# Performance work log

Hardware: AMD Instinct MI355X
Metric: run time of the kernel (lower is better)

The kernel has to match this reference:

```python
import jax, jax.numpy as jnp
import numpy as np

N_NODES = 50000
N_EDGES = 600000
D_FEAT = 128
HIDDEN = 128
N_CLASSES = 40
K_HOPS = 2


def setup_inputs() -> dict:
    key = jax.random.key(0)
    k_x, k_e, k_w1, k_b1, k_w2, k_b2 = jax.random.split(key, 6)
    x = jax.random.normal(k_x, (N_NODES, D_FEAT), dtype=jnp.float32)
    edge_index = jax.random.randint(k_e, (2, N_EDGES), 0, N_NODES, dtype=jnp.int64)
    # SGConv linear (applied after K-hop propagation) and classifier, Glorot-ish init
    W_sgc = jax.random.normal(k_w1, (D_FEAT, HIDDEN), dtype=jnp.float32) / np.sqrt(D_FEAT)
    b_sgc = jnp.zeros((HIDDEN,), dtype=jnp.float32)
    W_cls = jax.random.normal(k_w2, (HIDDEN, N_CLASSES), dtype=jnp.float32) / np.sqrt(HIDDEN)
    b_cls = jnp.zeros((N_CLASSES,), dtype=jnp.float32)
    return {"x": x, "edge_index": edge_index, "W_sgc": W_sgc, "b_sgc": b_sgc,
            "W_cls": W_cls, "b_cls": b_cls}


def _gcn_norm(edge_index, num_nodes):
    # Add self-loops (PyG SGConv default), compute symmetric GCN normalization.
    loops = jnp.arange(num_nodes, dtype=edge_index.dtype)
    src = jnp.concatenate([edge_index[0], loops])  # [E+N]
    dst = jnp.concatenate([edge_index[1], loops])  # [E+N]
    deg = jax.ops.segment_sum(jnp.ones_like(dst, dtype=jnp.float32), dst,
                              num_segments=num_nodes)
    dinv = jnp.where(deg > 0, jax.lax.rsqrt(deg), 0.0)
    norm = dinv[src] * dinv[dst]  # [E+N]
    return src, dst, norm


def reference(x, edge_index, W_sgc, b_sgc, W_cls, b_cls):
    num_nodes = x.shape[0]
    src, dst, norm = _gcn_norm(edge_index, num_nodes)
    h = x
    for _ in range(K_HOPS):  # K-hop propagation: h <- D^-1/2 (A+I) D^-1/2 h
        h = jax.ops.segment_sum(norm[:, None] * h[src], dst, num_segments=num_nodes)
    h = h @ W_sgc + b_sgc          # SGConv's trailing linear
    # F.dropout with training=False is identity (inference); skip.
    out = h @ W_cls + b_cls        # classifier
    return out
```

## Files before the change

### kernel.cpp

```cpp
#include <hip/hip_runtime.h>
#include <hip/hip_fp16.h>

#define N_NODES 50000
#define N_EDGES 600000
#define D 128
#define NC 40
#define BUCKET_CAP 48
#define NPART 8
#define PART_SZ (N_NODES / NPART)
#define E4 (N_EDGES / 4)
#define E4H (E4 / 2)
#define FUSE_ELEMS (D * NC + NC)

#define ZERO_BLKS ((N_NODES / 4 + 255) / 256)
#define FUSE_BLKS ((FUSE_ELEMS + 255) / 256)
#define CMP_BLKS ((E4 + 255) / 256)
#define K0B (ZERO_BLKS + FUSE_BLKS + CMP_BLKS)

#define K1B ((N_NODES + 63) / 64)
#define FTHR 192

#define PULLB ((N_NODES + 47) / 48)

typedef int v4i __attribute__((ext_vector_type(4)));
typedef _Float16 hf2 __attribute__((ext_vector_type(2)));

struct alignas(16) H8 { __half2 h[4]; };
struct alignas(8)  H4 { __half2 h[2]; };
struct alignas(16) HV4 { hf2 h[4]; };
struct alignas(8)  US4 { unsigned short s[4]; };

__device__ __forceinline__ float4 h4f(H4 v) {
    float2 p = __half22float2(v.h[0]), q = __half22float2(v.h[1]);
    return make_float4(p.x, p.y, q.x, q.y);
}


__global__ void k_prep(int4* __restrict__ cnt4,
                       const float* __restrict__ Wsgc, const float* __restrict__ bsgc,
                       const float* __restrict__ Wcls, const float* __restrict__ bcls,
                       float* __restrict__ Wf, float* __restrict__ bf,
                       const v4i* __restrict__ src4, const v4i* __restrict__ dst4,
                       v4i* __restrict__ packed4) {
    int b = blockIdx.x, t = threadIdx.x;
    if (b < ZERO_BLKS) {
        int i = b * 256 + t;
        if (i < N_NODES / 4) cnt4[i] = make_int4(0, 0, 0, 0);
    } else if (b < ZERO_BLKS + FUSE_BLKS) {
        int idx = (b - ZERO_BLKS) * 256 + t;
        if (idx < D * NC) {
            int k = idx / NC, c = idx % NC;
            float acc = 0.f;
            for (int j = 0; j < D; j++) acc += Wsgc[k * D + j] * Wcls[j * NC + c];
            Wf[idx] = acc;
        } else if (idx < FUSE_ELEMS) {
            int c = idx - D * NC;
            float acc = bcls[c];
            for (int j = 0; j < D; j++) acc += bsgc[j] * Wcls[j * NC + c];
            bf[c] = acc;
        }
    } else {
        int i = (b - ZERO_BLKS - FUSE_BLKS) * 256 + t;
        if (i < E4) {
            v4i d = __builtin_nontemporal_load(&dst4[i]);
            v4i s = __builtin_nontemporal_load(&src4[i]);
            v4i p;
            p.x = (int)(((unsigned)d.x << 16) | (unsigned)s.x);
            p.y = (int)(((unsigned)d.y << 16) | (unsigned)s.y);
            p.z = (int)(((unsigned)d.z << 16) | (unsigned)s.z);
            p.w = (int)(((unsigned)d.w << 16) | (unsigned)s.w);
            packed4[i] = p;
        }
    }
}


__device__ __forceinline__ void fill_range(const v4i* __restrict__ packed4,
                                           int* __restrict__ cnt,
                                           unsigned short* __restrict__ bucket,
                                           int gtid, int gstride,
                                           int i0, int i1, int lo, int hi) {
    for (int i = i0 + gtid; i < i1; i += gstride) {
        v4i p = packed4[i];
#define FO(pp)                                                             \
        {                                                                  \
            int d = (int)(((unsigned)(pp)) >> 16);                         \
            if (d >= lo && d < hi) {                                       \
                int pos = atomicAdd(&cnt[d], 1);                           \
                if (pos < BUCKET_CAP)                                      \
                    bucket[(size_t)d * BUCKET_CAP + pos] =                 \
                        (unsigned short)((pp) & 0xFFFF);                   \
            }                                                              \
        }
        FO(p.x) FO(p.y) FO(p.z) FO(p.w)
#undef FO
    }
}


__global__ __launch_bounds__(512) void k_fill_proj(
    const v4i* __restrict__ packed4, int* __restrict__ cnt,
    unsigned short* __restrict__ bucket,
    const float* __restrict__ x, const float* __restrict__ Wf,
    __half* __restrict__ z) {
    __shared__ hf2 sW[64][40];
    __shared__ hf2 sX[64][65];
    int t = threadIdx.x, b = blockIdx.x;
    int base = b * 64;

    int part = b & (NPART - 1);
    int nbip = (K1B - part + NPART - 1) / NPART;
    int bip  = b >> 3;
    int lo = part * PART_SZ, hi = lo + PART_SZ;
    int gtid = bip * FTHR + (t - 320);
    int gstride = nbip * FTHR;

    if (t >= 320) {
        fill_range(packed4, cnt, bucket, gtid, gstride, 0, E4H, lo, hi);
    } else {
        for (int i = t; i < 64 * 40; i += 320) {
            int k2 = i / 40, c = i - k2 * 40;
            hf2 w;
            w.x = (_Float16)Wf[(2 * k2) * NC + c];
            w.y = (_Float16)Wf[(2 * k2 + 1) * NC + c];
            sW[k2][c] = w;
        }
        int rows = N_NODES - base;
        if (rows > 64) rows = 64;
        const float4* xs4 = reinterpret_cast<const float4*>(x + (size_t)base * D);
        auto st4 = [&](int i, float4 v) {
            int r = i >> 5, k4 = i & 31;
            hf2 h0, h1;
            h0.x = (_Float16)v.x; h0.y = (_Float16)v.y;
            h1.x = (_Float16)v.z; h1.y = (_Float16)v.w;
            sX[r][2 * k4] = h0;
            sX[r][2 * k4 + 1] = h1;
        };
        if (rows == 64) {
            float4 r0 = xs4[t];
            float4 r1 = xs4[t + 320];
            float4 r2 = xs4[t + 640];
            float4 r3 = xs4[t + 960];
            float4 r4 = xs4[t + 1280];
            float4 r5 = xs4[t + 1600];
            float4 r6;
            bool has7 = (t < 128);
            if (has7) r6 = xs4[t + 1920];
            st4(t, r0); st4(t + 320, r1); st4(t + 640, r2); st4(t + 960, r3);
            st4(t + 1280, r4); st4(t + 1600, r5);
            if (has7) st4(t + 1920, r6);
        } else {
            for (int i = t; i < rows * 32; i += 320) st4(i, xs4[i]);
        }
    }
    __syncthreads();
    if (t >= 320) {
        fill_range(packed4, cnt, bucket, gtid, gstride, E4H, E4, lo, hi);
        return;
    }
    int lane = t & 63;
    int wv = t >> 6;
    int c0 = wv * 8;
    int node = base + lane;
    if (node >= N_NODES) return;
    float a0 = 0.f, a1 = 0.f, a2 = 0.f, a3 = 0.f;
    float a4 = 0.f, a5 = 0.f, a6 = 0.f, a7 = 0.f;
#pragma unroll 8
    for (int k2 = 0; k2 < 64; k2++) {
        hf2 hx = sX[lane][k2];
        HV4 wa = *reinterpret_cast<const HV4*>(&sW[k2][c0]);
        HV4 wb = *reinterpret_cast<const HV4*>(&sW[k2][c0 + 4]);
#if __has_builtin(__builtin_amdgcn_fdot2)
        a0 = __builtin_amdgcn_fdot2(hx, wa.h[0], a0, false);
        a1 = __builtin_amdgcn_fdot2(hx, wa.h[1], a1, false);
        a2 = __builtin_amdgcn_fdot2(hx, wa.h[2], a2, false);
        a3 = __builtin_amdgcn_fdot2(hx, wa.h[3], a3, false);
        a4 = __builtin_amdgcn_fdot2(hx, wb.h[0], a4, false);
        a5 = __builtin_amdgcn_fdot2(hx, wb.h[1], a5, false);
        a6 = __builtin_amdgcn_fdot2(hx, wb.h[2], a6, false);
        a7 = __builtin_amdgcn_fdot2(hx, wb.h[3], a7, false);
#else
        float xl = (float)hx.x, xh = (float)hx.y;
        a0 += xl * (float)wa.h[0].x + xh * (float)wa.h[0].y;
        a1 += xl * (float)wa.h[1].x + xh * (float)wa.h[1].y;
        a2 += xl * (float)wa.h[2].x + xh * (float)wa.h[2].y;
        a3 += xl * (float)wa.h[3].x + xh * (float)wa.h[3].y;
        a4 += xl * (float)wb.h[0].x + xh * (float)wb.h[0].y;
        a5 += xl * (float)wb.h[1].x + xh * (float)wb.h[1].y;
        a6 += xl * (float)wb.h[2].x + xh * (float)wb.h[2].y;
        a7 += xl * (float)wb.h[3].x + xh * (float)wb.h[3].y;
#endif
    }
    H8 o;
    o.h[0] = __floats2half2_rn(a0, a1);
    o.h[1] = __floats2half2_rn(a2, a3);
    o.h[2] = __floats2half2_rn(a4, a5);
    o.h[3] = __floats2half2_rn(a6, a7);
    *reinterpret_cast<H8*>(z + (size_t)node * NC + c0) = o;
}


template <int MODE>
__global__ __launch_bounds__(512) void k_pull(const int* __restrict__ cnt,
                                              const unsigned short* __restrict__ bucket,
                                              const __half* __restrict__ hin,
                                              void* __restrict__ houtv,
                                              const float* __restrict__ bias) {
    int wave = threadIdx.x >> 6;
    int lane = threadIdx.x & 63;
    int g = lane / 10;
    int l = lane - g * 10;
    int node = blockIdx.x * 48 + wave * 6 + g;
    if (g >= 6 || node >= N_NODES) return;
    int f = l << 2;
    int c = cnt[node];
    int n = c < BUCKET_CAP ? c : BUCKET_CAP;
    float di = rsqrtf((float)c + 1.0f);
    float4 acc = h4f(*reinterpret_cast<const H4*>(hin + (size_t)node * NC + f));
    if (MODE == 0) { acc.x *= di; acc.y *= di; acc.z *= di; acc.w *= di; }
    const unsigned short* bk = bucket + (size_t)node * BUCKET_CAP;
    int j = 0;
    for (; j + 4 <= n; j += 4) {
        US4 q = *reinterpret_cast<const US4*>(bk + j);
        int s0 = q.s[0], s1 = q.s[1], s2 = q.s[2], s3 = q.s[3];
        float4 v0 = h4f(*reinterpret_cast<const H4*>(hin + (size_t)s0 * NC + f));
        float4 v1 = h4f(*reinterpret_cast<const H4*>(hin + (size_t)s1 * NC + f));
        float4 v2 = h4f(*reinterpret_cast<const H4*>(hin + (size_t)s2 * NC + f));
        float4 v3 = h4f(*reinterpret_cast<const H4*>(hin + (size_t)s3 * NC + f));
        if (MODE == 0) {
            float w0 = rsqrtf((float)cnt[s0] + 1.0f);
            float w1 = rsqrtf((float)cnt[s1] + 1.0f);
            float w2 = rsqrtf((float)cnt[s2] + 1.0f);
            float w3 = rsqrtf((float)cnt[s3] + 1.0f);
            acc.x += w0 * v0.x + w1 * v1.x + w2 * v2.x + w3 * v3.x;
            acc.y += w0 * v0.y + w1 * v1.y + w2 * v2.y + w3 * v3.y;
            acc.z += w0 * v0.z + w1 * v1.z + w2 * v2.z + w3 * v3.z;
            acc.w += w0 * v0.w + w1 * v1.w + w2 * v2.w + w3 * v3.w;
        } else {
            acc.x += v0.x + v1.x + v2.x + v3.x;
            acc.y += v0.y + v1.y + v2.y + v3.y;
            acc.z += v0.z + v1.z + v2.z + v3.z;
            acc.w += v0.w + v1.w + v2.w + v3.w;
        }
    }
    for (; j < n; j++) {
        int s0 = bk[j];
        float4 v0 = h4f(*reinterpret_cast<const H4*>(hin + (size_t)s0 * NC + f));
        float w0 = (MODE == 0) ? rsqrtf((float)cnt[s0] + 1.0f) : 1.0f;
        acc.x += w0 * v0.x; acc.y += w0 * v0.y; acc.z += w0 * v0.z; acc.w += w0 * v0.w;
    }
    if (MODE == 0) {
        float sc = di * di;
        __half* ho = (__half*)houtv;
        H4 o;
        o.h[0] = __floats2half2_rn(sc * acc.x, sc * acc.y);
        o.h[1] = __floats2half2_rn(sc * acc.z, sc * acc.w);
        *reinterpret_cast<H4*>(ho + (size_t)node * NC + f) = o;
    } else {
        float* ho = (float*)houtv;
        float4 b = *reinterpret_cast<const float4*>(bias + f);
        acc.x = di * acc.x + b.x; acc.y = di * acc.y + b.y;
        acc.z = di * acc.z + b.z; acc.w = di * acc.w + b.w;
        *reinterpret_cast<float4*>(ho + (size_t)node * NC + f) = acc;
    }
}


extern "C" void kernel_launch(void* const* d_in, const int* in_sizes, int n_in,
                              void* d_out, int out_size, void* d_ws, size_t ws_size,
                              hipStream_t stream) {
    const float* x    = (const float*)d_in[0];
    const int*   ei   = (const int*)d_in[1];
    const float* Wsgc = (const float*)d_in[2];
    const float* bsgc = (const float*)d_in[3];
    const float* Wcls = (const float*)d_in[4];
    const float* bcls = (const float*)d_in[5];
    float* out = (float*)d_out;

    const v4i* src4 = (const v4i*)ei;
    const v4i* dst4 = (const v4i*)(ei + N_EDGES);

    char* ws = (char*)d_ws;
    size_t off = 0;
    auto alloc = [&](size_t bytes) -> void* {
        void* p = ws + off;
        off += (bytes + 255) & ~255ull;
        return p;
    };
    int*            cnt    = (int*)alloc((size_t)N_NODES * 4);
    unsigned short* bucket = (unsigned short*)alloc((size_t)N_NODES * BUCKET_CAP * 2);
    v4i*            packed = (v4i*)alloc((size_t)N_EDGES * 4);
    __half*         z      = (__half*)alloc((size_t)N_NODES * NC * 2);
    __half*         u1     = (__half*)alloc((size_t)N_NODES * NC * 2);
    float*          Wf     = (float*)alloc((size_t)D * NC * 4);
    float*          bf     = (float*)alloc((size_t)NC * 4);

    k_prep<<<K0B, 256, 0, stream>>>((int4*)cnt, Wsgc, bsgc, Wcls, bcls, Wf, bf,
                                    src4, dst4, (v4i*)packed);
    k_fill_proj<<<K1B, 512, 0, stream>>>((const v4i*)packed, cnt, bucket, x, Wf, z);
    k_pull<0><<<PULLB, 512, 0, stream>>>(cnt, bucket, z, (void*)u1, nullptr);
    k_pull<1><<<PULLB, 512, 0, stream>>>(cnt, bucket, u1, (void*)out, bf);
}
```

Baseline: 79.95 us.

## Drop edge packing pass and pad degree counters to separate cache lines

Removes the prep stage that packed src/dst into 16-bit pairs; the fill loop now reads the original int32 src and dst arrays directly. Degree counters are padded to a 64-byte stride so atomics on neighboring nodes do not share cache lines. In exchange, the partitioned fill rereads twice as many index bytes per pass, zeroing the counters takes more work, and the degree lookups in the pull kernels scatter across many more cache lines.

Result: slower. 96.74 us (+21.0%).

```diff
diff --git a/kernel.cpp b/kernel.cpp
--- a/kernel.cpp
+++ b/kernel.cpp
@@ -6,16 +6,17 @@
 #define D 128
 #define NC 40
 #define BUCKET_CAP 48
+#define CNT_STRIDE 16
 #define NPART 8
 #define PART_SZ (N_NODES / NPART)
 #define E4 (N_EDGES / 4)
 #define E4H (E4 / 2)
 #define FUSE_ELEMS (D * NC + NC)
 
-#define ZERO_BLKS ((N_NODES / 4 + 255) / 256)
+#define CNTI4 (N_NODES * CNT_STRIDE / 4)
+#define ZERO_BLKS ((CNTI4 + 255) / 256)
 #define FUSE_BLKS ((FUSE_ELEMS + 255) / 256)
-#define CMP_BLKS ((E4 + 255) / 256)
-#define K0B (ZERO_BLKS + FUSE_BLKS + CMP_BLKS)
+#define K0B (ZERO_BLKS + FUSE_BLKS)
 
 #define K1B ((N_NODES + 63) / 64)
 #define FTHR 192
@@ -39,14 +40,12 @@
 __global__ void k_prep(int4* __restrict__ cnt4,
                        const float* __restrict__ Wsgc, const float* __restrict__ bsgc,
                        const float* __restrict__ Wcls, const float* __restrict__ bcls,
-                       float* __restrict__ Wf, float* __restrict__ bf,
-                       const v4i* __restrict__ src4, const v4i* __restrict__ dst4,
-                       v4i* __restrict__ packed4) {
+                       float* __restrict__ Wf, float* __restrict__ bf) {
     int b = blockIdx.x, t = threadIdx.x;
     if (b < ZERO_BLKS) {
         int i = b * 256 + t;
-        if (i < N_NODES / 4) cnt4[i] = make_int4(0, 0, 0, 0);
-    } else if (b < ZERO_BLKS + FUSE_BLKS) {
+        if (i < CNTI4) cnt4[i] = make_int4(0, 0, 0, 0);
+    } else {
         int idx = (b - ZERO_BLKS) * 256 + t;
         if (idx < D * NC) {
             int k = idx / NC, c = idx % NC;
@@ -59,48 +58,38 @@
             for (int j = 0; j < D; j++) acc += bsgc[j] * Wcls[j * NC + c];
             bf[c] = acc;
         }
-    } else {
-        int i = (b - ZERO_BLKS - FUSE_BLKS) * 256 + t;
-        if (i < E4) {
-            v4i d = __builtin_nontemporal_load(&dst4[i]);
-            v4i s = __builtin_nontemporal_load(&src4[i]);
-            v4i p;
-            p.x = (int)(((unsigned)d.x << 16) | (unsigned)s.x);
-            p.y = (int)(((unsigned)d.y << 16) | (unsigned)s.y);
-            p.z = (int)(((unsigned)d.z << 16) | (unsigned)s.z);
-            p.w = (int)(((unsigned)d.w << 16) | (unsigned)s.w);
-            packed4[i] = p;
-        }
-    }
-}
-
-
-__device__ __forceinline__ void fill_range(const v4i* __restrict__ packed4,
+    }
+}
+
+
+__device__ __forceinline__ void fill_range(const v4i* __restrict__ src4,
+                                           const v4i* __restrict__ dst4,
                                            int* __restrict__ cnt,
                                            unsigned short* __restrict__ bucket,
                                            int gtid, int gstride,
                                            int i0, int i1, int lo, int hi) {
     for (int i = i0 + gtid; i < i1; i += gstride) {
-        v4i p = packed4[i];
-#define FO(pp)                                                             \
-        {                                                                  \
-            int d = (int)(((unsigned)(pp)) >> 16);                         \
-            if (d >= lo && d < hi) {                                       \
-                int pos = atomicAdd(&cnt[d], 1);                           \
-                if (pos < BUCKET_CAP)                                      \
-                    bucket[(size_t)d * BUCKET_CAP + pos] =                 \
-                        (unsigned short)((pp) & 0xFFFF);                   \
-            }                                                              \
-        }
-        FO(p.x) FO(p.y) FO(p.z) FO(p.w)
+        v4i d = __builtin_nontemporal_load(&dst4[i]);
+        v4i s = __builtin_nontemporal_load(&src4[i]);
+#define FO(dd, ss)                                                         \
+        if ((dd) >= lo && (dd) < hi) {                                     \
+            int pos = atomicAdd(&cnt[(size_t)(dd) * CNT_STRIDE], 1);       \
+            if (pos < BUCKET_CAP)                                          \
+                bucket[(size_t)(dd) * BUCKET_CAP + pos] =                  \
+                    (unsigned short)(ss);                                  \
+        }
+        FO(d.x, s.x)
+        FO(d.y, s.y)
+        FO(d.z, s.z)
+        FO(d.w, s.w)
 #undef FO
     }
 }
 
 
 __global__ __launch_bounds__(512) void k_fill_proj(
-    const v4i* __restrict__ packed4, int* __restrict__ cnt,
-    unsigned short* __restrict__ bucket,
+    const v4i* __restrict__ src4, const v4i* __restrict__ dst4,
+    int* __restrict__ cnt, unsigned short* __restrict__ bucket,
     const float* __restrict__ x, const float* __restrict__ Wf,
     __half* __restrict__ z) {
     __shared__ hf2 sW[64][40];
@@ -116,7 +105,7 @@
     int gstride = nbip * FTHR;
 
     if (t >= 320) {
-        fill_range(packed4, cnt, bucket, gtid, gstride, 0, E4H, lo, hi);
+        fill_range(src4, dst4, cnt, bucket, gtid, gstride, 0, E4H, lo, hi);
     } else {
         for (int i = t; i < 64 * 40; i += 320) {
             int k2 = i / 40, c = i - k2 * 40;
@@ -155,7 +144,7 @@
     }
     __syncthreads();
     if (t >= 320) {
-        fill_range(packed4, cnt, bucket, gtid, gstride, E4H, E4, lo, hi);
+        fill_range(src4, dst4, cnt, bucket, gtid, gstride, E4H, E4, lo, hi);
         return;
     }
     int lane = t & 63;
@@ -213,7 +202,7 @@
     int node = blockIdx.x * 48 + wave * 6 + g;
     if (g >= 6 || node >= N_NODES) return;
     int f = l << 2;
-    int c = cnt[node];
+    int c = cnt[(size_t)node * CNT_STRIDE];
     int n = c < BUCKET_CAP ? c : BUCKET_CAP;
     float di = rsqrtf((float)c + 1.0f);
     float4 acc = h4f(*reinterpret_cast<const H4*>(hin + (size_t)node * NC + f));
@@ -228,10 +217,10 @@
         float4 v2 = h4f(*reinterpret_cast<const H4*>(hin + (size_t)s2 * NC + f));
         float4 v3 = h4f(*reinterpret_cast<const H4*>(hin + (size_t)s3 * NC + f));
         if (MODE == 0) {
-            float w0 = rsqrtf((float)cnt[s0] + 1.0f);
-            float w1 = rsqrtf((float)cnt[s1] + 1.0f);
-            float w2 = rsqrtf((float)cnt[s2] + 1.0f);
-            float w3 = rsqrtf((float)cnt[s3] + 1.0f);
+            float w0 = rsqrtf((float)cnt[(size_t)s0 * CNT_STRIDE] + 1.0f);
+            float w1 = rsqrtf((float)cnt[(size_t)s1 * CNT_STRIDE] + 1.0f);
+            float w2 = rsqrtf((float)cnt[(size_t)s2 * CNT_STRIDE] + 1.0f);
+            float w3 = rsqrtf((float)cnt[(size_t)s3 * CNT_STRIDE] + 1.0f);
             acc.x += w0 * v0.x + w1 * v1.x + w2 * v2.x + w3 * v3.x;
             acc.y += w0 * v0.y + w1 * v1.y + w2 * v2.y + w3 * v3.y;
             acc.z += w0 * v0.z + w1 * v1.z + w2 * v2.z + w3 * v3.z;
@@ -246,7 +235,7 @@
     for (; j < n; j++) {
         int s0 = bk[j];
         float4 v0 = h4f(*reinterpret_cast<const H4*>(hin + (size_t)s0 * NC + f));
-        float w0 = (MODE == 0) ? rsqrtf((float)cnt[s0] + 1.0f) : 1.0f;
+        float w0 = (MODE == 0) ? rsqrtf((float)cnt[(size_t)s0 * CNT_STRIDE] + 1.0f) : 1.0f;
         acc.x += w0 * v0.x; acc.y += w0 * v0.y; acc.z += w0 * v0.z; acc.w += w0 * v0.w;
     }
     if (MODE == 0) {
@@ -287,17 +276,15 @@
         off += (bytes + 255) & ~255ull;
         return p;
     };
-    int*            cnt    = (int*)alloc((size_t)N_NODES * 4);
+    int*            cnt    = (int*)alloc((size_t)N_NODES * CNT_STRIDE * 4);
     unsigned short* bucket = (unsigned short*)alloc((size_t)N_NODES * BUCKET_CAP * 2);
-    v4i*            packed = (v4i*)alloc((size_t)N_EDGES * 4);
     __half*         z      = (__half*)alloc((size_t)N_NODES * NC * 2);
     __half*         u1     = (__half*)alloc((size_t)N_NODES * NC * 2);
     float*          Wf     = (float*)alloc((size_t)D * NC * 4);
     float*          bf     = (float*)alloc((size_t)NC * 4);
 
-    k_prep<<<K0B, 256, 0, stream>>>((int4*)cnt, Wsgc, bsgc, Wcls, bcls, Wf, bf,
-                                    src4, dst4, (v4i*)packed);
-    k_fill_proj<<<K1B, 512, 0, stream>>>((const v4i*)packed, cnt, bucket, x, Wf, z);
+    k_prep<<<K0B, 256, 0, stream>>>((int4*)cnt, Wsgc, bsgc, Wcls, bcls, Wf, bf);
+    k_fill_proj<<<K1B, 512, 0, stream>>>(src4, dst4, cnt, bucket, x, Wf, z);
     k_pull<0><<<PULLB, 512, 0, stream>>>(cnt, bucket, z, (void*)u1, nullptr);
     k_pull<1><<<PULLB, 512, 0, stream>>>(cnt, bucket, u1, (void*)out, bf);
 }
```
